# Kernel optimization log

Measured on AMD Instinct MI355X. Metric: run time of the kernel, lower is better.

The kernel has to match this reference:

```python
import jax, jax.numpy as jnp
import numpy as np

MESSAGE_PASSES = 3
HID = 100        # hidden_node_features == message_size
EDGE_F = 4       # n_edge_features
OUT = 100        # readout output dim


def setup_inputs() -> dict:
    key = jax.random.key(0)
    ks = jax.random.split(key, 8)
    B, N = 32, 128
    nodes = jax.random.normal(ks[0], (B, N, HID), dtype=jnp.float32)
    edges = jax.random.uniform(ks[1], (B, N, N, EDGE_F), dtype=jnp.float32)
    s = 1.0 / np.sqrt(HID)
    Wv = jax.random.normal(ks[2], (HID, HID), dtype=jnp.float32) * s
    Ww = jax.random.normal(ks[3], (HID, HID), dtype=jnp.float32) * s
    We = jax.random.normal(ks[4], (EDGE_F, HID), dtype=jnp.float32) * (1.0 / np.sqrt(EDGE_F))
    Wu = jax.random.normal(ks[5], (2 * HID, HID), dtype=jnp.float32) * (1.0 / np.sqrt(2 * HID))
    Wr = jax.random.normal(ks[6], (2 * HID, OUT), dtype=jnp.float32) * (1.0 / np.sqrt(2 * HID))
    return {"nodes": nodes, "edges": edges, "Wv": Wv, "Ww": Ww, "We": We, "Wu": Wu, "Wr": Wr}


def reference(nodes, edges, Wv, Ww, We, Wu, Wr):
    # adjacency[b,v,w] = sum_e edges[b,v,w,e]; nonzero entries define the edge set
    adjacency = edges.sum(axis=-1)                       # [B,N,N]
    edge_mask = adjacency != 0                           # [B,N,N]
    node_mask = adjacency.sum(axis=-1) != 0              # [B,N]

    # edge feature projection is constant across message passes
    e_proj = jnp.einsum('bvwe,eh->bvwh', edges, We)      # [B,N,N,H]

    hidden = nodes                                       # hidden_node_features == node feat dim
    for _ in range(MESSAGE_PASSES):
        # message_terms for every (b, v, w) edge: relu(h_v Wv + h_w Ww + e_vw We)
        pre = (hidden @ Wv)[:, :, None, :] + (hidden @ Ww)[:, None, :, :] + e_proj
        mterms = jnp.where(edge_mask[..., None], jax.nn.relu(pre), 0.0)
        # (same_batch * same_node) matmul == segment-sum over neighbors w
        messages = mterms.sum(axis=2)                    # [B,N,H]
        # update only nodes that appear in the edge set (degree > 0)
        upd = jnp.tanh(jnp.concatenate([hidden, messages], axis=-1) @ Wu)
        hidden = jnp.where(node_mask[..., None], upd, hidden)

    # readout: masked sum-pool of per-node graph terms
    graph_terms = jax.nn.relu(jnp.concatenate([hidden, nodes], axis=-1) @ Wr)  # [B,N,OUT]
    output = jnp.where(node_mask[..., None], graph_terms, 0.0).sum(axis=1)     # [B,OUT]
    return output
```

## Files before the change

### kernel.cpp

```cpp
#include <hip/hip_runtime.h>
#include <math.h>

#define B_   32
#define N_   128
#define H_   100
#define ROWS (B_ * N_)
#define RH   (ROWS * H_)

__global__ __launch_bounds__(256, 6) void k_proj0(const float* __restrict__ nodes,
                                                  const float* __restrict__ Wv,
                                                  const float* __restrict__ Ww,
                                                  float* __restrict__ hv,
                                                  float* __restrict__ hw) {
    __shared__ float nod_s[2][H_];
    const int row0 = blockIdx.x * 2;
    const int t = threadIdx.x, r = t >> 7, j = t & 127;
    {
        const float4* ng = (const float4*)(nodes + (size_t)row0 * H_);
        if (t < 50) ((float4*)nod_s)[t] = ng[t];
    }
    __syncthreads();
    if (j >= H_) return;
    const float4* h4p = (const float4*)nod_s[r];
    float va = 0.f, wa = 0.f;
#pragma unroll 5
    for (int k4 = 0; k4 < 25; ++k4) {
        const float4 h4 = h4p[k4];
        const int k = k4 * 4;
        va = fmaf(h4.x, Wv[(k + 0) * H_ + j], va);
        wa = fmaf(h4.x, Ww[(k + 0) * H_ + j], wa);
        va = fmaf(h4.y, Wv[(k + 1) * H_ + j], va);
        wa = fmaf(h4.y, Ww[(k + 1) * H_ + j], wa);
        va = fmaf(h4.z, Wv[(k + 2) * H_ + j], va);
        wa = fmaf(h4.z, Ww[(k + 2) * H_ + j], wa);
        va = fmaf(h4.w, Wv[(k + 3) * H_ + j], va);
        wa = fmaf(h4.w, Ww[(k + 3) * H_ + j], wa);
    }
    hv[(size_t)(row0 + r) * H_ + j] = va;
    hw[(size_t)(row0 + r) * H_ + j] = wa;
}

__global__ __launch_bounds__(256, 6) void k_pass(const float* __restrict__ edges,
                                                 const float* __restrict__ We,
                                                 const float* __restrict__ Wu,
                                                 const float* __restrict__ Wv,
                                                 const float* __restrict__ Ww,
                                                 const float* __restrict__ Wr,
                                                 const float* __restrict__ nodes,
                                                 float* __restrict__ hv_io,
                                                 const float* __restrict__ hw_in,
                                                 float* __restrict__ hw_out,
                                                 const float* __restrict__ hid_in,
                                                 float* __restrict__ hidden,
                                                 float* __restrict__ out,
                                                 int mode) {
    __shared__ float4 e_s[2][N_];
    __shared__ float  m_s[2][N_];
    __shared__ float  asum_part[4];
    __shared__ float  hid_s[2][H_];
    __shared__ float  msg_s[2][H_];
    __shared__ float  hn_s[2][H_];
    __shared__ float  nod_s[2][H_];
    __shared__ float  red_s[2][H_];

    const int row0 = blockIdx.x * 2;
    const int b = row0 >> 7;
    const int t = threadIdx.x, r = t >> 7, j = t & 127;
    const int wv = t >> 6, lane = t & 63;
    const int row = row0 + r;
    const bool act = (j < H_);

    {
        const float4* eg = (const float4*)(edges + (size_t)row0 * N_ * 4);
        const float4 e = eg[t];
        e_s[r][j] = e;
        float s = (e.x + e.y) + (e.z + e.w);
        m_s[r][j] = (s != 0.f) ? 1.f : 0.f;
#pragma unroll
        for (int off = 32; off > 0; off >>= 1) s += __shfl_down(s, off);
        if (lane == 0) asum_part[wv] = s;
    }
    {
        const float4* hg = (const float4*)(hid_in + (size_t)row0 * H_);
        if (t < 50) ((float4*)hid_s)[t] = hg[t];
        if (mode == 2) {
            const float4* ng = (const float4*)(nodes + (size_t)row0 * H_);
            if (t < 50) ((float4*)nod_s)[t] = ng[t];
        }
    }
    __syncthreads();

    const float nm = ((asum_part[2 * r] + asum_part[2 * r + 1]) != 0.f) ? 1.f : 0.f;

    if (act) {
        const float hvv = hv_io[(size_t)row * H_ + j];
        const float we0 = We[0 * H_ + j], we1 = We[1 * H_ + j];
        const float we2 = We[2 * H_ + j], we3 = We[3 * H_ + j];
        const float* hwp = hw_in + (size_t)b * N_ * H_ + j;
        float acc = 0.f;
#pragma unroll 8
        for (int w = 0; w < N_; ++w) {
            const float4 e = e_s[r][w];
            const float  m = m_s[r][w];
            const float  hww = hwp[w * H_];
            float p = hvv + hww;
            p = fmaf(e.x, we0, p);
            p = fmaf(e.y, we1, p);
            p = fmaf(e.z, we2, p);
            p = fmaf(e.w, we3, p);
            acc = fmaf(m, fmaxf(p, 0.f), acc);
        }
        msg_s[r][j] = acc;
    }
    __syncthreads();

    if (act) {
        const float4* h4p = (const float4*)hid_s[r];
        const float4* m4p = (const float4*)msg_s[r];
        float u = 0.f;
#pragma unroll 5
        for (int k4 = 0; k4 < 25; ++k4) {
            const float4 h4 = h4p[k4];
            const int k = k4 * 4;
            u = fmaf(h4.x, Wu[(k + 0) * H_ + j], u);
            u = fmaf(h4.y, Wu[(k + 1) * H_ + j], u);
            u = fmaf(h4.z, Wu[(k + 2) * H_ + j], u);
            u = fmaf(h4.w, Wu[(k + 3) * H_ + j], u);
        }
#pragma unroll 5
        for (int k4 = 0; k4 < 25; ++k4) {
            const float4 m4 = m4p[k4];
            const int k = H_ + k4 * 4;
            u = fmaf(m4.x, Wu[(k + 0) * H_ + j], u);
            u = fmaf(m4.y, Wu[(k + 1) * H_ + j], u);
            u = fmaf(m4.z, Wu[(k + 2) * H_ + j], u);
            u = fmaf(m4.w, Wu[(k + 3) * H_ + j], u);
        }
        const float nh = (nm != 0.f) ? tanhf(u) : hid_s[r][j];
        hn_s[r][j] = nh;
        if (mode == 1) hidden[(size_t)row * H_ + j] = nh;
    }
    __syncthreads();

    if (mode == 1) {
        if (act) {
            const float4* h4p = (const float4*)hn_s[r];
            float va = 0.f, wa = 0.f;
#pragma unroll 5
            for (int k4 = 0; k4 < 25; ++k4) {
                const float4 h4 = h4p[k4];
                const int k = k4 * 4;
                va = fmaf(h4.x, Wv[(k + 0) * H_ + j], va);
                wa = fmaf(h4.x, Ww[(k + 0) * H_ + j], wa);
                va = fmaf(h4.y, Wv[(k + 1) * H_ + j], va);
                wa = fmaf(h4.y, Ww[(k + 1) * H_ + j], wa);
                va = fmaf(h4.z, Wv[(k + 2) * H_ + j], va);
                wa = fmaf(h4.z, Ww[(k + 2) * H_ + j], wa);
                va = fmaf(h4.w, Wv[(k + 3) * H_ + j], va);
                wa = fmaf(h4.w, Ww[(k + 3) * H_ + j], wa);
            }
            hv_io[(size_t)row * H_ + j] = va;
            hw_out[(size_t)row * H_ + j] = wa;
        }
    } else {
        if (act) {
            const float4* h4p = (const float4*)hn_s[r];
            const float4* n4p = (const float4*)nod_s[r];
            float u = 0.f;
#pragma unroll 5
            for (int k4 = 0; k4 < 25; ++k4) {
                const float4 h4 = h4p[k4];
                const int k = k4 * 4;
                u = fmaf(h4.x, Wr[(k + 0) * H_ + j], u);
                u = fmaf(h4.y, Wr[(k + 1) * H_ + j], u);
                u = fmaf(h4.z, Wr[(k + 2) * H_ + j], u);
                u = fmaf(h4.w, Wr[(k + 3) * H_ + j], u);
            }
#pragma unroll 5
            for (int k4 = 0; k4 < 25; ++k4) {
                const float4 n4 = n4p[k4];
                const int k = H_ + k4 * 4;
                u = fmaf(n4.x, Wr[(k + 0) * H_ + j], u);
                u = fmaf(n4.y, Wr[(k + 1) * H_ + j], u);
                u = fmaf(n4.z, Wr[(k + 2) * H_ + j], u);
                u = fmaf(n4.w, Wr[(k + 3) * H_ + j], u);
            }
            red_s[r][j] = nm * fmaxf(u, 0.f);
        }
        __syncthreads();
        if (t < H_) atomicAdd(out + b * H_ + t, red_s[0][t] + red_s[1][t]);
    }
}

extern "C" void kernel_launch(void* const* d_in, const int* in_sizes, int n_in,
                              void* d_out, int out_size, void* d_ws, size_t ws_size,
                              hipStream_t stream) {
    const float* nodes = (const float*)d_in[0];
    const float* edges = (const float*)d_in[1];
    const float* Wv    = (const float*)d_in[2];
    const float* Ww    = (const float*)d_in[3];
    const float* We    = (const float*)d_in[4];
    const float* Wu    = (const float*)d_in[5];
    const float* Wr    = (const float*)d_in[6];
    float* out = (float*)d_out;

    float* hidden = (float*)d_ws;
    float* hv     = hidden + RH;
    float* hwA    = hv + RH;
    float* hwB    = hwA + RH;

    hipMemsetAsync(d_out, 0, (size_t)out_size * sizeof(float), stream);

    k_proj0<<<ROWS / 2, 256, 0, stream>>>(nodes, Wv, Ww, hv, hwA);

    k_pass<<<ROWS / 2, 256, 0, stream>>>(edges, We, Wu, Wv, Ww, Wr, nodes,
                                         hv, hwA, hwB, nodes, hidden, out, 1);
    k_pass<<<ROWS / 2, 256, 0, stream>>>(edges, We, Wu, Wv, Ww, Wr, nodes,
                                         hv, hwB, hwA, hidden, hidden, out, 1);
    k_pass<<<ROWS / 2, 256, 0, stream>>>(edges, We, Wu, Wv, Ww, Wr, nodes,
                                         hv, hwA, hwB, hidden, hidden, out, 2);
}
```

Before: 196.3 us.

## Map each row to one wavefront with two hidden columns per lane

The pass kernel now launches 128 threads per block, one 64-lane wavefront per node row, and each lane computes two hidden columns (l and l+64). Previously 128 lanes served 100 columns, so 28 lanes per row sat idle. The edge mask and node-degree sum are now computed inside the neighbour loop instead of a separate shared-memory and shuffle stage. The readout atomics are issued per lane directly, with no shared reduction. This removes idle lanes and some barriers, but doubles per-lane serial work and halves threads per block, which may cut latency hiding. Lanes with no second column redundantly load and compute column 99.

```diff
diff --git a/kernel.cpp b/kernel.cpp
--- a/kernel.cpp
+++ b/kernel.cpp
@@ -40,7 +40,7 @@
     hw[(size_t)(row0 + r) * H_ + j] = wa;
 }
 
-__global__ __launch_bounds__(256, 6) void k_pass(const float* __restrict__ edges,
+__global__ __launch_bounds__(128, 8) void k_pass(const float* __restrict__ edges,
                                                  const float* __restrict__ We,
                                                  const float* __restrict__ Wu,
                                                  const float* __restrict__ Wv,
@@ -55,140 +55,167 @@
                                                  float* __restrict__ out,
                                                  int mode) {
     __shared__ float4 e_s[2][N_];
-    __shared__ float  m_s[2][N_];
-    __shared__ float  asum_part[4];
     __shared__ float  hid_s[2][H_];
     __shared__ float  msg_s[2][H_];
     __shared__ float  hn_s[2][H_];
     __shared__ float  nod_s[2][H_];
-    __shared__ float  red_s[2][H_];
 
     const int row0 = blockIdx.x * 2;
     const int b = row0 >> 7;
-    const int t = threadIdx.x, r = t >> 7, j = t & 127;
-    const int wv = t >> 6, lane = t & 63;
-    const int row = row0 + r;
-    const bool act = (j < H_);
+    const int t = threadIdx.x, wv = t >> 6, l = t & 63;
+    const int row = row0 + wv;
 
     {
         const float4* eg = (const float4*)(edges + (size_t)row0 * N_ * 4);
-        const float4 e = eg[t];
-        e_s[r][j] = e;
-        float s = (e.x + e.y) + (e.z + e.w);
-        m_s[r][j] = (s != 0.f) ? 1.f : 0.f;
-#pragma unroll
-        for (int off = 32; off > 0; off >>= 1) s += __shfl_down(s, off);
-        if (lane == 0) asum_part[wv] = s;
-    }
-    {
+        ((float4*)e_s)[t]       = eg[t];
+        ((float4*)e_s)[t + 128] = eg[t + 128];
         const float4* hg = (const float4*)(hid_in + (size_t)row0 * H_);
         if (t < 50) ((float4*)hid_s)[t] = hg[t];
-        if (mode == 2) {
-            const float4* ng = (const float4*)(nodes + (size_t)row0 * H_);
-            if (t < 50) ((float4*)nod_s)[t] = ng[t];
-        }
-    }
-    __syncthreads();
-
-    const float nm = ((asum_part[2 * r] + asum_part[2 * r + 1]) != 0.f) ? 1.f : 0.f;
-
-    if (act) {
-        const float hvv = hv_io[(size_t)row * H_ + j];
-        const float we0 = We[0 * H_ + j], we1 = We[1 * H_ + j];
-        const float we2 = We[2 * H_ + j], we3 = We[3 * H_ + j];
-        const float* hwp = hw_in + (size_t)b * N_ * H_ + j;
-        float acc = 0.f;
-#pragma unroll 8
+        if (mode == 2 && t < 50)
+            ((float4*)nod_s)[t] = ((const float4*)(nodes + (size_t)row0 * H_))[t];
+    }
+    __syncthreads();
+
+    const int h0 = l;
+    const bool a1 = (l < H_ - 64);
+    const int h1 = a1 ? (l + 64) : (H_ - 1);
+
+    const float hv0 = hv_io[(size_t)row * H_ + h0];
+    const float hv1 = hv_io[(size_t)row * H_ + h1];
+    const float we00 = We[0 * H_ + h0], we01 = We[1 * H_ + h0];
+    const float we02 = We[2 * H_ + h0], we03 = We[3 * H_ + h0];
+    const float we10 = We[0 * H_ + h1], we11 = We[1 * H_ + h1];
+    const float we12 = We[2 * H_ + h1], we13 = We[3 * H_ + h1];
+
+    float acc0 = 0.f, acc1 = 0.f, asum = 0.f;
+    {
+        const float* hp = hw_in + (size_t)b * N_ * H_;
+#pragma unroll 4
         for (int w = 0; w < N_; ++w) {
-            const float4 e = e_s[r][w];
-            const float  m = m_s[r][w];
-            const float  hww = hwp[w * H_];
-            float p = hvv + hww;
-            p = fmaf(e.x, we0, p);
-            p = fmaf(e.y, we1, p);
-            p = fmaf(e.z, we2, p);
-            p = fmaf(e.w, we3, p);
-            acc = fmaf(m, fmaxf(p, 0.f), acc);
-        }
-        msg_s[r][j] = acc;
-    }
-    __syncthreads();
-
-    if (act) {
-        const float4* h4p = (const float4*)hid_s[r];
-        const float4* m4p = (const float4*)msg_s[r];
-        float u = 0.f;
+            const float4 e = e_s[wv][w];
+            const float hw0 = hp[h0];
+            const float hw1 = hp[h1];
+            hp += H_;
+            const float s = (e.x + e.y) + (e.z + e.w);
+            asum += s;
+            const float m = (s != 0.f) ? 1.f : 0.f;
+            float p0 = hv0 + hw0, p1 = hv1 + hw1;
+            p0 = fmaf(e.x, we00, p0); p1 = fmaf(e.x, we10, p1);
+            p0 = fmaf(e.y, we01, p0); p1 = fmaf(e.y, we11, p1);
+            p0 = fmaf(e.z, we02, p0); p1 = fmaf(e.z, we12, p1);
+            p0 = fmaf(e.w, we03, p0); p1 = fmaf(e.w, we13, p1);
+            acc0 = fmaf(m, fmaxf(p0, 0.f), acc0);
+            acc1 = fmaf(m, fmaxf(p1, 0.f), acc1);
+        }
+    }
+    msg_s[wv][h0] = acc0;
+    if (a1) msg_s[wv][l + 64] = acc1;
+    __syncthreads();
+
+    const float nm = (asum != 0.f) ? 1.f : 0.f;
+    float u0 = 0.f, u1 = 0.f;
+    {
+        const float4* h4p = (const float4*)hid_s[wv];
+        const float4* m4p = (const float4*)msg_s[wv];
 #pragma unroll 5
         for (int k4 = 0; k4 < 25; ++k4) {
             const float4 h4 = h4p[k4];
             const int k = k4 * 4;
-            u = fmaf(h4.x, Wu[(k + 0) * H_ + j], u);
-            u = fmaf(h4.y, Wu[(k + 1) * H_ + j], u);
-            u = fmaf(h4.z, Wu[(k + 2) * H_ + j], u);
-            u = fmaf(h4.w, Wu[(k + 3) * H_ + j], u);
+            u0 = fmaf(h4.x, Wu[(k + 0) * H_ + h0], u0);
+            u1 = fmaf(h4.x, Wu[(k + 0) * H_ + h1], u1);
+            u0 = fmaf(h4.y, Wu[(k + 1) * H_ + h0], u0);
+            u1 = fmaf(h4.y, Wu[(k + 1) * H_ + h1], u1);
+            u0 = fmaf(h4.z, Wu[(k + 2) * H_ + h0], u0);
+            u1 = fmaf(h4.z, Wu[(k + 2) * H_ + h1], u1);
+            u0 = fmaf(h4.w, Wu[(k + 3) * H_ + h0], u0);
+            u1 = fmaf(h4.w, Wu[(k + 3) * H_ + h1], u1);
         }
 #pragma unroll 5
         for (int k4 = 0; k4 < 25; ++k4) {
             const float4 m4 = m4p[k4];
             const int k = H_ + k4 * 4;
-            u = fmaf(m4.x, Wu[(k + 0) * H_ + j], u);
-            u = fmaf(m4.y, Wu[(k + 1) * H_ + j], u);
-            u = fmaf(m4.z, Wu[(k + 2) * H_ + j], u);
-            u = fmaf(m4.w, Wu[(k + 3) * H_ + j], u);
-        }
-        const float nh = (nm != 0.f) ? tanhf(u) : hid_s[r][j];
-        hn_s[r][j] = nh;
-        if (mode == 1) hidden[(size_t)row * H_ + j] = nh;
-    }
-    __syncthreads();
-
+            u0 = fmaf(m4.x, Wu[(k + 0) * H_ + h0], u0);
+            u1 = fmaf(m4.x, Wu[(k + 0) * H_ + h1], u1);
+            u0 = fmaf(m4.y, Wu[(k + 1) * H_ + h0], u0);
+            u1 = fmaf(m4.y, Wu[(k + 1) * H_ + h1], u1);
+            u0 = fmaf(m4.z, Wu[(k + 2) * H_ + h0], u0);
+            u1 = fmaf(m4.z, Wu[(k + 2) * H_ + h1], u1);
+            u0 = fmaf(m4.w, Wu[(k + 3) * H_ + h0], u0);
+            u1 = fmaf(m4.w, Wu[(k + 3) * H_ + h1], u1);
+        }
+    }
+    const float nh0 = (nm != 0.f) ? tanhf(u0) : hid_s[wv][h0];
+    const float nh1 = (nm != 0.f) ? tanhf(u1) : hid_s[wv][h1];
+    hn_s[wv][h0] = nh0;
+    if (a1) hn_s[wv][l + 64] = nh1;
     if (mode == 1) {
-        if (act) {
-            const float4* h4p = (const float4*)hn_s[r];
-            float va = 0.f, wa = 0.f;
-#pragma unroll 5
-            for (int k4 = 0; k4 < 25; ++k4) {
-                const float4 h4 = h4p[k4];
-                const int k = k4 * 4;
-                va = fmaf(h4.x, Wv[(k + 0) * H_ + j], va);
-                wa = fmaf(h4.x, Ww[(k + 0) * H_ + j], wa);
-                va = fmaf(h4.y, Wv[(k + 1) * H_ + j], va);
-                wa = fmaf(h4.y, Ww[(k + 1) * H_ + j], wa);
-                va = fmaf(h4.z, Wv[(k + 2) * H_ + j], va);
-                wa = fmaf(h4.z, Ww[(k + 2) * H_ + j], wa);
-                va = fmaf(h4.w, Wv[(k + 3) * H_ + j], va);
-                wa = fmaf(h4.w, Ww[(k + 3) * H_ + j], wa);
-            }
-            hv_io[(size_t)row * H_ + j] = va;
-            hw_out[(size_t)row * H_ + j] = wa;
+        hidden[(size_t)row * H_ + h0] = nh0;
+        if (a1) hidden[(size_t)row * H_ + l + 64] = nh1;
+    }
+    __syncthreads();
+
+    if (mode == 1) {
+        const float4* h4p = (const float4*)hn_s[wv];
+        float va0 = 0, va1 = 0, wa0 = 0, wa1 = 0;
+#pragma unroll 5
+        for (int k4 = 0; k4 < 25; ++k4) {
+            const float4 h4 = h4p[k4];
+            const int k = k4 * 4;
+            va0 = fmaf(h4.x, Wv[(k + 0) * H_ + h0], va0);
+            va1 = fmaf(h4.x, Wv[(k + 0) * H_ + h1], va1);
+            wa0 = fmaf(h4.x, Ww[(k + 0) * H_ + h0], wa0);
+            wa1 = fmaf(h4.x, Ww[(k + 0) * H_ + h1], wa1);
+            va0 = fmaf(h4.y, Wv[(k + 1) * H_ + h0], va0);
+            va1 = fmaf(h4.y, Wv[(k + 1) * H_ + h1], va1);
+            wa0 = fmaf(h4.y, Ww[(k + 1) * H_ + h0], wa0);
+            wa1 = fmaf(h4.y, Ww[(k + 1) * H_ + h1], wa1);
+            va0 = fmaf(h4.z, Wv[(k + 2) * H_ + h0], va0);
+            va1 = fmaf(h4.z, Wv[(k + 2) * H_ + h1], va1);
+            wa0 = fmaf(h4.z, Ww[(k + 2) * H_ + h0], wa0);
+            wa1 = fmaf(h4.z, Ww[(k + 2) * H_ + h1], wa1);
+            va0 = fmaf(h4.w, Wv[(k + 3) * H_ + h0], va0);
+            va1 = fmaf(h4.w, Wv[(k + 3) * H_ + h1], va1);
+            wa0 = fmaf(h4.w, Ww[(k + 3) * H_ + h0], wa0);
+            wa1 = fmaf(h4.w, Ww[(k + 3) * H_ + h1], wa1);
+        }
+        hv_io[(size_t)row * H_ + h0] = va0;
+        hw_out[(size_t)row * H_ + h0] = wa0;
+        if (a1) {
+            hv_io[(size_t)row * H_ + l + 64] = va1;
+            hw_out[(size_t)row * H_ + l + 64] = wa1;
         }
     } else {
-        if (act) {
-            const float4* h4p = (const float4*)hn_s[r];
-            const float4* n4p = (const float4*)nod_s[r];
-            float u = 0.f;
-#pragma unroll 5
-            for (int k4 = 0; k4 < 25; ++k4) {
-                const float4 h4 = h4p[k4];
-                const int k = k4 * 4;
-                u = fmaf(h4.x, Wr[(k + 0) * H_ + j], u);
-                u = fmaf(h4.y, Wr[(k + 1) * H_ + j], u);
-                u = fmaf(h4.z, Wr[(k + 2) * H_ + j], u);
-                u = fmaf(h4.w, Wr[(k + 3) * H_ + j], u);
-            }
-#pragma unroll 5
-            for (int k4 = 0; k4 < 25; ++k4) {
-                const float4 n4 = n4p[k4];
-                const int k = H_ + k4 * 4;
-                u = fmaf(n4.x, Wr[(k + 0) * H_ + j], u);
-                u = fmaf(n4.y, Wr[(k + 1) * H_ + j], u);
-                u = fmaf(n4.z, Wr[(k + 2) * H_ + j], u);
-                u = fmaf(n4.w, Wr[(k + 3) * H_ + j], u);
-            }
-            red_s[r][j] = nm * fmaxf(u, 0.f);
-        }
-        __syncthreads();
-        if (t < H_) atomicAdd(out + b * H_ + t, red_s[0][t] + red_s[1][t]);
+        const float4* h4p = (const float4*)hn_s[wv];
+        const float4* n4p = (const float4*)nod_s[wv];
+        float r0 = 0.f, r1 = 0.f;
+#pragma unroll 5
+        for (int k4 = 0; k4 < 25; ++k4) {
+            const float4 h4 = h4p[k4];
+            const int k = k4 * 4;
+            r0 = fmaf(h4.x, Wr[(k + 0) * H_ + h0], r0);
+            r1 = fmaf(h4.x, Wr[(k + 0) * H_ + h1], r1);
+            r0 = fmaf(h4.y, Wr[(k + 1) * H_ + h0], r0);
+            r1 = fmaf(h4.y, Wr[(k + 1) * H_ + h1], r1);
+            r0 = fmaf(h4.z, Wr[(k + 2) * H_ + h0], r0);
+            r1 = fmaf(h4.z, Wr[(k + 2) * H_ + h1], r1);
+            r0 = fmaf(h4.w, Wr[(k + 3) * H_ + h0], r0);
+            r1 = fmaf(h4.w, Wr[(k + 3) * H_ + h1], r1);
+        }
+#pragma unroll 5
+        for (int k4 = 0; k4 < 25; ++k4) {
+            const float4 n4 = n4p[k4];
+            const int k = H_ + k4 * 4;
+            r0 = fmaf(n4.x, Wr[(k + 0) * H_ + h0], r0);
+            r1 = fmaf(n4.x, Wr[(k + 0) * H_ + h1], r1);
+            r0 = fmaf(n4.y, Wr[(k + 1) * H_ + h0], r0);
+            r1 = fmaf(n4.y, Wr[(k + 1) * H_ + h1], r1);
+            r0 = fmaf(n4.z, Wr[(k + 2) * H_ + h0], r0);
+            r1 = fmaf(n4.z, Wr[(k + 2) * H_ + h1], r1);
+            r0 = fmaf(n4.w, Wr[(k + 3) * H_ + h0], r0);
+            r1 = fmaf(n4.w, Wr[(k + 3) * H_ + h1], r1);
+        }
+        atomicAdd(out + b * H_ + h0, nm * fmaxf(r0, 0.f));
+        if (a1) atomicAdd(out + b * H_ + l + 64, nm * fmaxf(r1, 0.f));
     }
 }
 
@@ -213,10 +240,10 @@
 
     k_proj0<<<ROWS / 2, 256, 0, stream>>>(nodes, Wv, Ww, hv, hwA);
 
-    k_pass<<<ROWS / 2, 256, 0, stream>>>(edges, We, Wu, Wv, Ww, Wr, nodes,
+    k_pass<<<ROWS / 2, 128, 0, stream>>>(edges, We, Wu, Wv, Ww, Wr, nodes,
                                          hv, hwA, hwB, nodes, hidden, out, 1);
-    k_pass<<<ROWS / 2, 256, 0, stream>>>(edges, We, Wu, Wv, Ww, Wr, nodes,
+    k_pass<<<ROWS / 2, 128, 0, stream>>>(edges, We, Wu, Wv, Ww, Wr, nodes,
                                          hv, hwB, hwA, hidden, hidden, out, 1);
-    k_pass<<<ROWS / 2, 256, 0, stream>>>(edges, We, Wu, Wv, Ww, Wr, nodes,
+    k_pass<<<ROWS / 2, 128, 0, stream>>>(edges, We, Wu, Wv, Ww, Wr, nodes,
                                          hv, hwA, hwB, hidden, hidden, out, 2);
 }
```

New measurement: 289.8 us. +47.7%, slower.

## Remap message loop: split neighbors across waves, two features per lane

Applied to the files above, without the earlier changes.

The message aggregation is reassigned so each wave handles one row and half of the neighbor range, with each lane computing two adjacent hidden features through float2 loads. This raises the active lanes from 100 of 128 per row to 50 of 64 per wave, loads hw with wider accesses and halves the serial loop length. The edge mask and adjacency sum are now computed inside the loop rather than in a separate prologue. In exchange it adds a shared-memory partial-sum buffer, an extra barrier and a reduction step.

```diff
diff --git a/kernel.cpp b/kernel.cpp
--- a/kernel.cpp
+++ b/kernel.cpp
@@ -55,64 +55,69 @@
                                                  float* __restrict__ out,
                                                  int mode) {
     __shared__ float4 e_s[2][N_];
-    __shared__ float  m_s[2][N_];
-    __shared__ float  asum_part[4];
     __shared__ float  hid_s[2][H_];
+    __shared__ float  msgp_s[4][H_];
     __shared__ float  msg_s[2][H_];
     __shared__ float  hn_s[2][H_];
     __shared__ float  nod_s[2][H_];
     __shared__ float  red_s[2][H_];
+    __shared__ float  asum_s[4];
 
     const int row0 = blockIdx.x * 2;
     const int b = row0 >> 7;
     const int t = threadIdx.x, r = t >> 7, j = t & 127;
-    const int wv = t >> 6, lane = t & 63;
+    const int wv = t >> 6, l = t & 63;
+    const int rw = wv >> 1;
+    const int half = wv & 1;
+    const int roww = row0 + rw;
     const int row = row0 + r;
     const bool act = (j < H_);
+    const bool mact = (l < 50);
+    const int ll = mact ? l : 49;
 
     {
         const float4* eg = (const float4*)(edges + (size_t)row0 * N_ * 4);
-        const float4 e = eg[t];
-        e_s[r][j] = e;
-        float s = (e.x + e.y) + (e.z + e.w);
-        m_s[r][j] = (s != 0.f) ? 1.f : 0.f;
-#pragma unroll
-        for (int off = 32; off > 0; off >>= 1) s += __shfl_down(s, off);
-        if (lane == 0) asum_part[wv] = s;
-    }
-    {
+        ((float4*)e_s)[t] = eg[t];
         const float4* hg = (const float4*)(hid_in + (size_t)row0 * H_);
         if (t < 50) ((float4*)hid_s)[t] = hg[t];
-        if (mode == 2) {
-            const float4* ng = (const float4*)(nodes + (size_t)row0 * H_);
-            if (t < 50) ((float4*)nod_s)[t] = ng[t];
-        }
-    }
-    __syncthreads();
-
-    const float nm = ((asum_part[2 * r] + asum_part[2 * r + 1]) != 0.f) ? 1.f : 0.f;
-
-    if (act) {
-        const float hvv = hv_io[(size_t)row * H_ + j];
-        const float we0 = We[0 * H_ + j], we1 = We[1 * H_ + j];
-        const float we2 = We[2 * H_ + j], we3 = We[3 * H_ + j];
-        const float* hwp = hw_in + (size_t)b * N_ * H_ + j;
-        float acc = 0.f;
+        if (mode == 2 && t < 50)
+            ((float4*)nod_s)[t] = ((const float4*)(nodes + (size_t)row0 * H_))[t];
+    }
+    __syncthreads();
+
+    {
+        const float2 hv2 = *(const float2*)(hv_io + (size_t)roww * H_ + 2 * ll);
+        const float2 we0 = *(const float2*)(We + 0 * H_ + 2 * ll);
+        const float2 we1 = *(const float2*)(We + 1 * H_ + 2 * ll);
+        const float2 we2 = *(const float2*)(We + 2 * H_ + 2 * ll);
+        const float2 we3 = *(const float2*)(We + 3 * H_ + 2 * ll);
+        const int w0 = half * 64;
+        const float* hwbase = hw_in + ((size_t)b * N_ + w0) * H_ + 2 * ll;
+        float acc0 = 0.f, acc1 = 0.f, asum = 0.f;
 #pragma unroll 8
-        for (int w = 0; w < N_; ++w) {
-            const float4 e = e_s[r][w];
-            const float  m = m_s[r][w];
-            const float  hww = hwp[w * H_];
-            float p = hvv + hww;
-            p = fmaf(e.x, we0, p);
-            p = fmaf(e.y, we1, p);
-            p = fmaf(e.z, we2, p);
-            p = fmaf(e.w, we3, p);
-            acc = fmaf(m, fmaxf(p, 0.f), acc);
-        }
-        msg_s[r][j] = acc;
-    }
-    __syncthreads();
+        for (int w = 0; w < 64; ++w) {
+            const float4 e = e_s[rw][w0 + w];
+            const float2 hw2 = *(const float2*)(hwbase + w * H_);
+            const float s = (e.x + e.y) + (e.z + e.w);
+            asum += s;
+            const float m = (s != 0.f) ? 1.f : 0.f;
+            float p0 = hv2.x + hw2.x, p1 = hv2.y + hw2.y;
+            p0 = fmaf(e.x, we0.x, p0); p1 = fmaf(e.x, we0.y, p1);
+            p0 = fmaf(e.y, we1.x, p0); p1 = fmaf(e.y, we1.y, p1);
+            p0 = fmaf(e.z, we2.x, p0); p1 = fmaf(e.z, we2.y, p1);
+            p0 = fmaf(e.w, we3.x, p0); p1 = fmaf(e.w, we3.y, p1);
+            acc0 = fmaf(m, fmaxf(p0, 0.f), acc0);
+            acc1 = fmaf(m, fmaxf(p1, 0.f), acc1);
+        }
+        if (mact) *(float2*)(&msgp_s[wv][2 * l]) = make_float2(acc0, acc1);
+        if (l == 0) asum_s[wv] = asum;
+    }
+    __syncthreads();
+
+    if (act) msg_s[r][j] = msgp_s[2 * r][j] + msgp_s[2 * r + 1][j];
+    __syncthreads();
+
+    const float nm = ((asum_s[2 * r] + asum_s[2 * r + 1]) != 0.f) ? 1.f : 0.f;
 
     if (act) {
         const float4* h4p = (const float4*)hid_s[r];
```

New measurement: 214.5 us. +9.3%, slower.
